# Performance work log

Measured on AMD Instinct MI355X. Metric: run time of the kernel, lower is better.

The kernel has to match this reference:

```python
import jax, jax.numpy as jnp
import numpy as np

INFEAT = 4096
OUTFEAT = 11008
TOKENS = 2048


def setup_inputs() -> dict:
    key = jax.random.key(0)
    k1, k2, k3, k4, k5 = jax.random.split(key, 5)
    x = jax.random.normal(k1, (TOKENS, INFEAT), dtype=jnp.float32)
    # Random uint8 int-weights, packed 4-per-uint32 exactly like pack():
    # word = w1 | w2<<8 | w3<<16 | w4<<24, rows grouped along infeatures.
    wbytes = jax.random.randint(k2, (INFEAT // 4, 4, OUTFEAT), 0, 256, dtype=jnp.int32).astype(jnp.uint32)
    qweight = (wbytes[:, 0] | (wbytes[:, 1] << 8) | (wbytes[:, 2] << 16) | (wbytes[:, 3] << 24))
    qweight = qweight.astype(jnp.int32)  # same bit pattern as uint32 buffer
    scales = (jax.random.uniform(k3, (OUTFEAT,), dtype=jnp.float32) * 0.01 + 1e-4)
    zeros = jax.random.randint(k4, (OUTFEAT,), 0, 256, dtype=jnp.int32)  # uint8 zero points
    bias = jax.random.normal(k5, (OUTFEAT,), dtype=jnp.float32) * 0.01
    return {"x": x, "qweight": qweight, "scales": scales, "zeros": zeros, "bias": bias}


def _dequant(qweight, scales, zeros):
    q = qweight.astype(jnp.uint32)  # [INFEAT//4, OUTFEAT]
    b0 = (q & 0xFF)
    b1 = ((q >> 8) & 0xFF)
    b2 = ((q >> 16) & 0xFF)
    b3 = ((q >> 24) & 0xFF)
    w_int = jnp.stack([b0, b1, b2, b3], axis=1).reshape(-1, q.shape[-1])  # [INFEAT, OUTFEAT]
    # pack(): int = round(w/scale) + zero  =>  w = (int - zero) * scale (per output channel)
    return (w_int.astype(jnp.float32) - zeros.astype(jnp.float32)[None, :]) * scales[None, :]


def reference(x, qweight, scales, zeros, bias):
    w = _dequant(qweight, scales, zeros)          # [INFEAT, OUTFEAT]
    return x @ w + bias[None, :]                  # [TOKENS, OUTFEAT]
```

## Files before the change

kernel.cpp:

```cpp
#include <hip/hip_runtime.h>
#include <hip/hip_bf16.h>

#define INFEAT 4096
#define OUTFEAT 11008
#define TOKENS 2048

typedef int v4i __attribute__((ext_vector_type(4)));
typedef __bf16 bf16_t;
typedef bf16_t bf16x4 __attribute__((ext_vector_type(4)));
typedef bf16_t bf16x8 __attribute__((ext_vector_type(8)));
typedef float f32x4 __attribute__((ext_vector_type(4)));

__device__ __forceinline__ void async_copy16(const void* g, void* l) {
    __builtin_amdgcn_global_load_lds((const __attribute__((address_space(1))) void*)g,
                                     (__attribute__((address_space(3))) void*)l,
                                     16, 0, 0);
}

__global__ __launch_bounds__(256) void prep(
    const float* __restrict__ x, const unsigned int* __restrict__ qw,
    unsigned int* __restrict__ xq, float* __restrict__ xscale, int* __restrict__ xsum,
    unsigned char* __restrict__ wt)
{
    __shared__ unsigned int Tw[64 * 64];
    __shared__ float smax[4];
    __shared__ int ssum[4];
    const int tid = threadIdx.x;

    if (blockIdx.x < 2752) {
        const int bid = blockIdx.x;
        const int n0  = (bid % 172) * 64;
        const int kp0 = (bid / 172) * 64;
        const int tn4 = tid & 15;
        const int kb  = tid >> 4;
        #pragma unroll
        for (int it = 0; it < 4; ++it) {
            const int kp = kb + it * 16;
            uint4 q = *(const uint4*)&qw[(size_t)(kp0 + kp) * OUTFEAT + n0 + tn4 * 4];
            q.x ^= 0x80808080u; q.y ^= 0x80808080u; q.z ^= 0x80808080u; q.w ^= 0x80808080u;
            const int ks = kp >> 2, kq = kp & 3;
            const int n = tn4 * 4;
            Tw[(n + 0) * 64 + ((ks ^ ((n + 0) & 15)) << 2) + kq] = q.x;
            Tw[(n + 1) * 64 + ((ks ^ ((n + 1) & 15)) << 2) + kq] = q.y;
            Tw[(n + 2) * 64 + ((ks ^ ((n + 2) & 15)) << 2) + kq] = q.z;
            Tw[(n + 3) * 64 + ((ks ^ ((n + 3) & 15)) << 2) + kq] = q.w;
        }
        __syncthreads();
        #pragma unroll
        for (int i = 0; i < 4; ++i) {
            const int flat = i * 256 + tid;
            const int n = flat >> 4;
            const int c = flat & 15;
            uint4 v = *(const uint4*)&Tw[n * 64 + ((c ^ (n & 15)) * 4)];
            *(uint4*)&wt[(size_t)(n0 + n) * INFEAT + (size_t)kp0 * 4 + c * 16] = v;
        }
    } else {
        const int row = blockIdx.x - 2752;
        const int lane = tid & 63, wid = tid >> 6;
        const float* xr = x + (size_t)row * INFEAT;

        float4 v[4];
        #pragma unroll
        for (int i = 0; i < 4; ++i) v[i] = *(const float4*)&xr[tid * 16 + i * 4];

        float am = 0.f;
        #pragma unroll
        for (int i = 0; i < 4; ++i)
            am = fmaxf(am, fmaxf(fmaxf(fabsf(v[i].x), fabsf(v[i].y)),
                                 fmaxf(fabsf(v[i].z), fabsf(v[i].w))));
        #pragma unroll
        for (int o = 32; o > 0; o >>= 1) am = fmaxf(am, __shfl_xor(am, o, 64));
        if (lane == 0) smax[wid] = am;
        __syncthreads();
        am = fmaxf(fmaxf(smax[0], smax[1]), fmaxf(smax[2], smax[3]));
        const float inv = am > 0.f ? 127.0f / am : 0.f;
        const float sc  = am > 0.f ? am / 127.0f : 0.f;

        int lsum = 0;
        unsigned int pk[4];
        #pragma unroll
        for (int i = 0; i < 4; ++i) {
            int q0 = (int)rintf(fminf(fmaxf(v[i].x * inv, -127.f), 127.f));
            int q1 = (int)rintf(fminf(fmaxf(v[i].y * inv, -127.f), 127.f));
            int q2 = (int)rintf(fminf(fmaxf(v[i].z * inv, -127.f), 127.f));
            int q3 = (int)rintf(fminf(fmaxf(v[i].w * inv, -127.f), 127.f));
            lsum += q0 + q1 + q2 + q3;
            pk[i] = (q0 & 255) | ((q1 & 255) << 8) | ((q2 & 255) << 16) | ((unsigned)(q3 & 255) << 24);
        }
        *(uint4*)&xq[(size_t)row * (INFEAT / 4) + tid * 4] = *(uint4*)pk;

        #pragma unroll
        for (int o = 32; o > 0; o >>= 1) lsum += __shfl_xor(lsum, o, 64);
        if (lane == 0) ssum[wid] = lsum;
        __syncthreads();
        if (tid == 0) {
            xsum[row] = ssum[0] + ssum[1] + ssum[2] + ssum[3];
            xscale[row] = sc;
        }
    }
}

__global__ __launch_bounds__(256, 2) void q3gemm_i8d(
    const unsigned char* __restrict__ xqb, const unsigned char* __restrict__ wt,
    const float* __restrict__ scales, const int* __restrict__ zeros,
    const float* __restrict__ bias, const float* __restrict__ xscale,
    const int* __restrict__ xsum, float* __restrict__ out)
{
    __shared__ unsigned char Als[2][128 * 128];
    __shared__ unsigned char Bls[2][128 * 128];

    const int tid = threadIdx.x;
    const int sbid = (blockIdx.x & 7) * 172 + (blockIdx.x >> 3);
    const int n0 = (sbid >> 4) * 128;
    const int m0 = (sbid & 15) * 128;

    const int wid = tid >> 6, lane = tid & 63;
    const int wm = (wid & 1) * 64, wn = (wid >> 1) * 64;
    const int lr = lane & 15, lq = lane >> 4;

    const int rb0  = wid * 32;
    const int rsub = lane >> 3;
    const int sl   = lane & 7;

    v4i acc[4][4];
    #pragma unroll
    for (int i = 0; i < 4; ++i)
        #pragma unroll
        for (int j = 0; j < 4; ++j)
            acc[i][j] = (v4i){0, 0, 0, 0};

#define STAGE(T, C) do {                                                              \
    const int kk0_ = (T) * 128;                                                       \
    _Pragma("unroll")                                                                 \
    for (int p_ = 0; p_ < 4; ++p_) {                                                  \
        const int r_ = rb0 + p_ * 8 + rsub;                                           \
        const int s_ = sl ^ (r_ & 7);                                                 \
        async_copy16(&xqb[(size_t)(m0 + r_) * INFEAT + kk0_ + s_ * 16],               \
                     &Als[C][(rb0 + p_ * 8) * 128]);                                  \
    }                                                                                 \
    _Pragma("unroll")                                                                 \
    for (int p_ = 0; p_ < 4; ++p_) {                                                  \
        const int r_ = rb0 + p_ * 8 + rsub;                                           \
        const int s_ = sl ^ (r_ & 7);                                                 \
        async_copy16(&wt[(size_t)(n0 + r_) * INFEAT + kk0_ + s_ * 16],                \
                     &Bls[C][(rb0 + p_ * 8) * 128]);                                  \
    }                                                                                 \
} while (0)

    const int NT = INFEAT / 128;

    STAGE(0, 0);
    STAGE(1, 1);
    asm volatile("s_waitcnt vmcnt(8)" ::: "memory");
    __builtin_amdgcn_sched_barrier(0);
    __builtin_amdgcn_s_barrier();
    __builtin_amdgcn_sched_barrier(0);

    for (int t = 0; t < NT; ++t) {
        const int cur = t & 1;
        const unsigned char* Ab = Als[cur];
        const unsigned char* Bb = Bls[cur];

        v4i af[2][4], bfv[2][4];
        #pragma unroll
        for (int ks = 0; ks < 2; ++ks)
            #pragma unroll
            for (int q = 0; q < 4; ++q) {
                const int ra = wm + q * 16 + lr;
                const int pa = (ks * 4 + lq) ^ (ra & 7);
                af[ks][q] = *(const v4i*)&Ab[ra * 128 + pa * 16];
                const int rb = wn + q * 16 + lr;
                const int pb = (ks * 4 + lq) ^ (rb & 7);
                bfv[ks][q] = *(const v4i*)&Bb[rb * 128 + pb * 16];
            }
        asm volatile("s_waitcnt lgkmcnt(0)" ::: "memory");
        __builtin_amdgcn_sched_barrier(0);
        __builtin_amdgcn_s_barrier();
        __builtin_amdgcn_sched_barrier(0);

        if (t + 2 < NT) STAGE(t + 2, cur);

        #pragma unroll
        for (int ks = 0; ks < 2; ++ks)
            #pragma unroll
            for (int i = 0; i < 4; ++i)
                #pragma unroll
                for (int j = 0; j < 4; ++j)
                    acc[i][j] = __builtin_amdgcn_mfma_i32_16x16x64_i8(af[ks][i], bfv[ks][j], acc[i][j], 0, 0, 0);

        __builtin_amdgcn_sched_barrier(0);
        if (t < NT - 2) { asm volatile("s_waitcnt vmcnt(8)" ::: "memory"); }
        else            { asm volatile("s_waitcnt vmcnt(0)" ::: "memory"); }
        __builtin_amdgcn_sched_barrier(0);
        __builtin_amdgcn_s_barrier();
        __builtin_amdgcn_sched_barrier(0);
    }
#undef STAGE

    #pragma unroll
    for (int j = 0; j < 4; ++j) {
        const int col = n0 + wn + j * 16 + lr;
        const float sn = scales[col];
        const int zi = 128 - zeros[col];
        const float bv = bias[col];
        #pragma unroll
        for (int i = 0; i < 4; ++i) {
            const int rb = m0 + wm + i * 16 + lq * 4;
            #pragma unroll
            for (int r = 0; r < 4; ++r) {
                const int tot = acc[i][j][r] + zi * xsum[rb + r];
                out[(size_t)(rb + r) * OUTFEAT + col] = xscale[rb + r] * sn * (float)tot + bv;
            }
        }
    }
}

#define LDSS 72
__global__ __launch_bounds__(256) void q3gemm_fb(
    const float* __restrict__ x, const unsigned int* __restrict__ qw,
    const float* __restrict__ scales, const int* __restrict__ zeros,
    const float* __restrict__ bias, float* __restrict__ out)
{
    __shared__ bf16_t Als[128 * LDSS];
    __shared__ bf16_t Bls[128 * LDSS];
    const int tid = threadIdx.x;
    const int m0 = blockIdx.y * 128;
    const int n0 = blockIdx.x * 128;
    const int bcol = tid & 127;
    const int bpr  = tid >> 7;
    const float scf = scales[n0 + bcol];
    const float nzs = (float)zeros[n0 + bcol] * scf;
    const int acolg = tid & 15;
    const int arow0 = tid >> 4;
    const int wid  = tid >> 6;
    const int lane = tid & 63;
    const int wm = (wid & 1) * 64;
    const int wn = (wid >> 1) * 64;
    const int lr = lane & 15;
    const int lq = lane >> 4;
    f32x4 acc[4][4];
    #pragma unroll
    for (int i = 0; i < 4; ++i)
        #pragma unroll
        for (int j = 0; j < 4; ++j) acc[i][j] = (f32x4)0.0f;
    for (int kt = 0; kt < INFEAT / 64; ++kt) {
        const int k0 = kt * 64;
        #pragma unroll
        for (int p = 0; p < 8; ++p) {
            const int row = arow0 + p * 16;
            const float4 v = *(const float4*)&x[(size_t)(m0 + row) * INFEAT + k0 + acolg * 4];
            bf16x4 b;
            b[0] = (bf16_t)v.x; b[1] = (bf16_t)v.y; b[2] = (bf16_t)v.z; b[3] = (bf16_t)v.w;
            *(bf16x4*)&Als[row * LDSS + acolg * 4] = b;
        }
        const int kp0 = k0 >> 2;
        #pragma unroll
        for (int it = 0; it < 8; ++it) {
            const int prel = it * 2 + bpr;
            const unsigned int q = qw[(size_t)(kp0 + prel) * OUTFEAT + n0 + bcol];
            bf16x4 b;
            b[0] = (bf16_t)((float)(q & 0xFFu)        * scf - nzs);
            b[1] = (bf16_t)((float)((q >> 8) & 0xFFu) * scf - nzs);
            b[2] = (bf16_t)((float)((q >> 16) & 0xFFu)* scf - nzs);
            b[3] = (bf16_t)((float)(q >> 24)          * scf - nzs);
            *(bf16x4*)&Bls[bcol * LDSS + prel * 4] = b;
        }
        __syncthreads();
        #pragma unroll
        for (int ks = 0; ks < 2; ++ks) {
            bf16x8 af[4], bfv[4];
            #pragma unroll
            for (int t = 0; t < 4; ++t) {
                af[t]  = *(const bf16x8*)&Als[(wm + t * 16 + lr) * LDSS + ks * 32 + lq * 8];
                bfv[t] = *(const bf16x8*)&Bls[(wn + t * 16 + lr) * LDSS + ks * 32 + lq * 8];
            }
            #pragma unroll
            for (int i = 0; i < 4; ++i)
                #pragma unroll
                for (int j = 0; j < 4; ++j)
                    acc[i][j] = __builtin_amdgcn_mfma_f32_16x16x32_bf16(af[i], bfv[j], acc[i][j], 0, 0, 0);
        }
        __syncthreads();
    }
    #pragma unroll
    for (int j = 0; j < 4; ++j) {
        const int col = n0 + wn + j * 16 + lr;
        const float bv = bias[col];
        #pragma unroll
        for (int i = 0; i < 4; ++i) {
            const int rbs = m0 + wm + i * 16 + lq * 4;
            #pragma unroll
            for (int r = 0; r < 4; ++r)
                out[(size_t)(rbs + r) * OUTFEAT + col] = acc[i][j][r] + bv;
        }
    }
}

extern "C" void kernel_launch(void* const* d_in, const int* in_sizes, int n_in,
                              void* d_out, int out_size, void* d_ws, size_t ws_size,
                              hipStream_t stream) {
    const float*        x      = (const float*)d_in[0];
    const unsigned int* qw     = (const unsigned int*)d_in[1];
    const float*        scales = (const float*)d_in[2];
    const int*          zeros  = (const int*)d_in[3];
    const float*        bias   = (const float*)d_in[4];
    float*              out    = (float*)d_out;

    const size_t wt_bytes = (size_t)OUTFEAT * INFEAT;
    const size_t xq_bytes = (size_t)TOKENS * INFEAT;
    const size_t need = wt_bytes + xq_bytes + TOKENS * (sizeof(float) + sizeof(int)) + 256;

    if (ws_size >= need) {
        unsigned char* wt = (unsigned char*)d_ws;
        unsigned int* xq  = (unsigned int*)((char*)d_ws + wt_bytes);
        float* xscale = (float*)((char*)d_ws + wt_bytes + xq_bytes);
        int*   xsum   = (int*)((char*)d_ws + wt_bytes + xq_bytes + TOKENS * sizeof(float));

        prep<<<dim3(2752 + TOKENS), dim3(256), 0, stream>>>(x, qw, xq, xscale, xsum, wt);
        q3gemm_i8d<<<dim3((OUTFEAT / 128) * (TOKENS / 128)), dim3(256), 0, stream>>>(
            (const unsigned char*)xq, wt, scales, zeros, bias, xscale, xsum, out);
    } else {
        q3gemm_fb<<<dim3(OUTFEAT / 128, TOKENS / 128), dim3(256), 0, stream>>>(
            x, qw, scales, zeros, bias, out);
    }
}
```

Measured before the change: 266.7 us.

## Halve K-tile to 64 for higher occupancy and drop block swizzle

Shrinks the int8 GEMM K-tile from 128 to 64 bytes, cutting shared memory per block from 64KB to 32KB and raising the launch-bounds occupancy target from 2 to 4 blocks per CU. The LDS XOR swizzle is redone for 4 chunks per row, and the wait counts are adjusted. The blockIdx remapping that grouped tiles for L2 locality is replaced with a plain linear mapping. More resident blocks should hide latency better, at the cost of twice as many barriers and pipeline iterations, fewer MFMAs between syncs, and possibly worse cache reuse.

```diff
diff --git a/kernel.cpp b/kernel.cpp
--- a/kernel.cpp
+++ b/kernel.cpp
@@ -100,27 +100,26 @@
     }
 }
 
-__global__ __launch_bounds__(256, 2) void q3gemm_i8d(
+__global__ __launch_bounds__(256, 4) void q3gemm_i8e(
     const unsigned char* __restrict__ xqb, const unsigned char* __restrict__ wt,
     const float* __restrict__ scales, const int* __restrict__ zeros,
     const float* __restrict__ bias, const float* __restrict__ xscale,
     const int* __restrict__ xsum, float* __restrict__ out)
 {
-    __shared__ unsigned char Als[2][128 * 128];
-    __shared__ unsigned char Bls[2][128 * 128];
+    __shared__ unsigned char Als[2][128 * 64];
+    __shared__ unsigned char Bls[2][128 * 64];
 
     const int tid = threadIdx.x;
-    const int sbid = (blockIdx.x & 7) * 172 + (blockIdx.x >> 3);
-    const int n0 = (sbid >> 4) * 128;
-    const int m0 = (sbid & 15) * 128;
+    const int n0 = (blockIdx.x >> 4) * 128;
+    const int m0 = (blockIdx.x & 15) * 128;
 
     const int wid = tid >> 6, lane = tid & 63;
     const int wm = (wid & 1) * 64, wn = (wid >> 1) * 64;
     const int lr = lane & 15, lq = lane >> 4;
 
-    const int rb0  = wid * 32;
-    const int rsub = lane >> 3;
-    const int sl   = lane & 7;
+    const int rb0 = wid * 32;
+    const int rs  = lane >> 2;
+    const int sl  = lane & 3;
 
     v4i acc[4][4];
     #pragma unroll
@@ -130,28 +129,28 @@
             acc[i][j] = (v4i){0, 0, 0, 0};
 
 #define STAGE(T, C) do {                                                              \
-    const int kk0_ = (T) * 128;                                                       \
+    const int kk0_ = (T) * 64;                                                        \
     _Pragma("unroll")                                                                 \
-    for (int p_ = 0; p_ < 4; ++p_) {                                                  \
-        const int r_ = rb0 + p_ * 8 + rsub;                                           \
-        const int s_ = sl ^ (r_ & 7);                                                 \
+    for (int p_ = 0; p_ < 2; ++p_) {                                                  \
+        const int r_ = rb0 + p_ * 16 + rs;                                            \
+        const int s_ = sl ^ ((r_ + (r_ >> 2)) & 3);                                   \
         async_copy16(&xqb[(size_t)(m0 + r_) * INFEAT + kk0_ + s_ * 16],               \
-                     &Als[C][(rb0 + p_ * 8) * 128]);                                  \
+                     &Als[C][(rb0 + p_ * 16) * 64]);                                  \
     }                                                                                 \
     _Pragma("unroll")                                                                 \
-    for (int p_ = 0; p_ < 4; ++p_) {                                                  \
-        const int r_ = rb0 + p_ * 8 + rsub;                                           \
-        const int s_ = sl ^ (r_ & 7);                                                 \
+    for (int p_ = 0; p_ < 2; ++p_) {                                                  \
+        const int r_ = rb0 + p_ * 16 + rs;                                            \
+        const int s_ = sl ^ ((r_ + (r_ >> 2)) & 3);                                   \
         async_copy16(&wt[(size_t)(n0 + r_) * INFEAT + kk0_ + s_ * 16],                \
-                     &Bls[C][(rb0 + p_ * 8) * 128]);                                  \
+                     &Bls[C][(rb0 + p_ * 16) * 64]);                                  \
     }                                                                                 \
 } while (0)
 
-    const int NT = INFEAT / 128;
+    const int NT = INFEAT / 64;
 
     STAGE(0, 0);
     STAGE(1, 1);
-    asm volatile("s_waitcnt vmcnt(8)" ::: "memory");
+    asm volatile("s_waitcnt vmcnt(4)" ::: "memory");
     __builtin_amdgcn_sched_barrier(0);
     __builtin_amdgcn_s_barrier();
     __builtin_amdgcn_sched_barrier(0);
@@ -161,18 +160,16 @@
         const unsigned char* Ab = Als[cur];
         const unsigned char* Bb = Bls[cur];
 
-        v4i af[2][4], bfv[2][4];
-        #pragma unroll
-        for (int ks = 0; ks < 2; ++ks)
-            #pragma unroll
-            for (int q = 0; q < 4; ++q) {
-                const int ra = wm + q * 16 + lr;
-                const int pa = (ks * 4 + lq) ^ (ra & 7);
-                af[ks][q] = *(const v4i*)&Ab[ra * 128 + pa * 16];
-                const int rb = wn + q * 16 + lr;
-                const int pb = (ks * 4 + lq) ^ (rb & 7);
-                bfv[ks][q] = *(const v4i*)&Bb[rb * 128 + pb * 16];
-            }
+        v4i af[4], bfv[4];
+        #pragma unroll
+        for (int q = 0; q < 4; ++q) {
+            const int ra = wm + q * 16 + lr;
+            const int pa = lq ^ ((ra + (ra >> 2)) & 3);
+            af[q] = *(const v4i*)&Ab[ra * 64 + pa * 16];
+            const int rb = wn + q * 16 + lr;
+            const int pb = lq ^ ((rb + (rb >> 2)) & 3);
+            bfv[q] = *(const v4i*)&Bb[rb * 64 + pb * 16];
+        }
         asm volatile("s_waitcnt lgkmcnt(0)" ::: "memory");
         __builtin_amdgcn_sched_barrier(0);
         __builtin_amdgcn_s_barrier();
@@ -181,15 +178,13 @@
         if (t + 2 < NT) STAGE(t + 2, cur);
 
         #pragma unroll
-        for (int ks = 0; ks < 2; ++ks)
-            #pragma unroll
-            for (int i = 0; i < 4; ++i)
-                #pragma unroll
-                for (int j = 0; j < 4; ++j)
-                    acc[i][j] = __builtin_amdgcn_mfma_i32_16x16x64_i8(af[ks][i], bfv[ks][j], acc[i][j], 0, 0, 0);
-
-        __builtin_amdgcn_sched_barrier(0);
-        if (t < NT - 2) { asm volatile("s_waitcnt vmcnt(8)" ::: "memory"); }
+        for (int i = 0; i < 4; ++i)
+            #pragma unroll
+            for (int j = 0; j < 4; ++j)
+                acc[i][j] = __builtin_amdgcn_mfma_i32_16x16x64_i8(af[i], bfv[j], acc[i][j], 0, 0, 0);
+
+        __builtin_amdgcn_sched_barrier(0);
+        if (t < NT - 2) { asm volatile("s_waitcnt vmcnt(4)" ::: "memory"); }
         else            { asm volatile("s_waitcnt vmcnt(0)" ::: "memory"); }
         __builtin_amdgcn_sched_barrier(0);
         __builtin_amdgcn_s_barrier();
@@ -317,7 +312,7 @@
         int*   xsum   = (int*)((char*)d_ws + wt_bytes + xq_bytes + TOKENS * sizeof(float));
 
         prep<<<dim3(2752 + TOKENS), dim3(256), 0, stream>>>(x, qw, xq, xscale, xsum, wt);
-        q3gemm_i8d<<<dim3((OUTFEAT / 128) * (TOKENS / 128)), dim3(256), 0, stream>>>(
+        q3gemm_i8e<<<dim3((OUTFEAT / 128) * (TOKENS / 128)), dim3(256), 0, stream>>>(
             (const unsigned char*)xq, wt, scales, zeros, bias, xscale, xsum, out);
     } else {
         q3gemm_fb<<<dim3(OUTFEAT / 128, TOKENS / 128), dim3(256), 0, stream>>>(
```

Measured after the change: 308.4 us. +15.6%, slower.
